# Performance work log

Hardware: AMD Instinct MI355X
Metric: run time of the kernel (lower is better)

Reference implementation:

```python
import jax, jax.numpy as jnp
import numpy as np

BN_EPS = 1e-5

def _segment_mean(vals, idx, num_segments):
    s = jax.ops.segment_sum(vals, idx, num_segments=num_segments)
    cnt = jax.ops.segment_sum(jnp.ones((vals.shape[0],), vals.dtype), idx, num_segments=num_segments)
    return s / jnp.maximum(cnt, 1.0)[:, None]


def setup_inputs() -> dict:
    N, E, L = 50000, 800000, 1600000
    ND, ED = 256, 128
    key = jax.random.key(0)
    ks = jax.random.split(key, 8)
    return {
        "x": jax.random.normal(ks[0], (N, ND), jnp.float32),
        "edge_attr": jax.random.normal(ks[1], (E, ED), jnp.float32),
        "W_proj": jax.random.normal(ks[2], (ED, ND), jnp.float32) / np.sqrt(ND),
        "W1": jax.random.normal(ks[3], (ED, ED), jnp.float32) / np.sqrt(ED),
        "b1": jnp.zeros((ED,), jnp.float32),
        "prelu_a": jnp.full((1,), 0.25, jnp.float32),
        "bn_gamma": jnp.ones((ED,), jnp.float32),
        "bn_beta": jnp.zeros((ED,), jnp.float32),
        "edge_index": jax.random.randint(ks[4], (2, E), 0, N, jnp.int32),
        "line_graph_edge_index": jax.random.randint(ks[5], (2, L), 0, E, jnp.int32),
    }


def reference(x, edge_attr, W_proj, W1, b1, prelu_a, bn_gamma, bn_beta, edge_index, line_graph_edge_index):
    N = x.shape[0]
    E = edge_attr.shape[0]
    src, dst = edge_index[0], edge_index[1]
    # project once then gather (same math as gathering then projecting)
    px = x @ W_proj.T  # [N, edge_dim]
    fused = edge_attr + (px[src] + px[dst]) * 0.5  # [E, edge_dim]
    # line-graph message passing: scatter-mean over destination edges
    line_src, line_dst = line_graph_edge_index[0], line_graph_edge_index[1]
    agg = _segment_mean(fused[line_src], line_dst, E)  # [E, edge_dim]
    # edge update: Linear -> PReLU -> BatchNorm1d (training-mode batch stats)
    h = agg @ W1.T + b1
    h = jnp.where(h >= 0, h, prelu_a * h)
    mean = jnp.mean(h, axis=0)
    var = jnp.mean(jnp.square(h - mean), axis=0)  # biased, as torch BN
    h = (h - mean) * jax.lax.rsqrt(var + BN_EPS) * bn_gamma + bn_beta
    fused = fused + h
    # aggregate edges back to nodes (scatter-mean over dst)
    node_updates = _segment_mean(fused, dst, N)  # [N, edge_dim]
    return node_updates
```

## Files before the change

kernel.cpp:

```cpp
#include <hip/hip_runtime.h>
#include <cstdint>

#define BN_EPS 1e-5f

typedef __attribute__((ext_vector_type(8))) short bf16x8;
typedef __attribute__((ext_vector_type(4))) float f32x4;

#define GLD16(dst, src)                                                        \
  __builtin_amdgcn_global_load_lds(                                            \
      (const __attribute__((address_space(1))) void*)(src),                    \
      (__attribute__((address_space(3))) void*)(dst), 16, 0, 0)

__device__ inline void split8(const float* f, bf16x8& hi, bf16x8& lo) {
#pragma unroll
  for (int j = 0; j < 8; ++j) {
    unsigned u = __float_as_uint(f[j]);
    hi[j] = (short)(u >> 16);
    float r = f[j] - __uint_as_float(u & 0xFFFF0000u);
    lo[j] = (short)(__float_as_uint(r) >> 16);
  }
}

template<int K, bool EPI>
__global__ __launch_bounds__(256) void gemm_kernel(
    const float* __restrict__ A,
    const float* __restrict__ W,
    const float* __restrict__ bias,
    const float* __restrict__ prelu_a,
    float* __restrict__ C,
    float* __restrict__ bnsum,
    float* __restrict__ bnsumsq,
    int M)
{
    constexpr int BM = 64, BN = 128, BK = 32;
    __shared__ float aT[BK][BM + 4];
    __shared__ float wT[BK][BN];

    const int tid = threadIdx.x;
    const int tx = tid & 31;
    const int ty = tid >> 5;
    const int row0 = blockIdx.x * BM;

    float acc[8][4];
#pragma unroll
    for (int r = 0; r < 8; ++r)
#pragma unroll
        for (int c = 0; c < 4; ++c) acc[r][c] = 0.f;

    for (int k0 = 0; k0 < K; k0 += BK) {
#pragma unroll
        for (int rep = 0; rep < 2; ++rep) {
            int r  = (tid >> 3) + rep * 32;
            int kq = tid & 7;
            int grow = row0 + r;
            float4 v = make_float4(0.f, 0.f, 0.f, 0.f);
            if (grow < M)
                v = *(const float4*)(A + (size_t)grow * K + k0 + 4 * kq);
            aT[4*kq+0][r] = v.x;
            aT[4*kq+1][r] = v.y;
            aT[4*kq+2][r] = v.z;
            aT[4*kq+3][r] = v.w;
        }
#pragma unroll
        for (int rep = 0; rep < 4; ++rep) {
            int j  = tid & 127;
            int kh = tid >> 7;
            int kk = kh * 16 + rep * 4;
            float4 v = *(const float4*)(W + (size_t)j * K + k0 + kk);
            wT[kk+0][j] = v.x;
            wT[kk+1][j] = v.y;
            wT[kk+2][j] = v.z;
            wT[kk+3][j] = v.w;
        }
        __syncthreads();
#pragma unroll
        for (int k = 0; k < BK; ++k) {
            float4 w4 = *(const float4*)&wT[k][4*tx];
            float4 a0 = *(const float4*)&aT[k][8*ty];
            float4 a1 = *(const float4*)&aT[k][8*ty+4];
            float av[8] = {a0.x,a0.y,a0.z,a0.w,a1.x,a1.y,a1.z,a1.w};
            float wv[4] = {w4.x,w4.y,w4.z,w4.w};
#pragma unroll
            for (int r = 0; r < 8; ++r)
#pragma unroll
                for (int c = 0; c < 4; ++c)
                    acc[r][c] = fmaf(av[r], wv[c], acc[r][c]);
        }
        __syncthreads();
    }

#pragma unroll
    for (int r = 0; r < 8; ++r) {
        int grow = row0 + 8*ty + r;
        if (grow < M) {
            float4 o = make_float4(acc[r][0], acc[r][1], acc[r][2], acc[r][3]);
            *(float4*)(C + (size_t)grow * BN + 4*tx) = o;
        }
    }
    (void)bias; (void)prelu_a; (void)bnsum; (void)bnsumsq;
}

__global__ __launch_bounds__(512, 1) void gemm_h_kernel(
    const float* __restrict__ A,
    const float* __restrict__ W,
    const float* __restrict__ bias,
    const float* __restrict__ prelu_a,
    float* __restrict__ C,
    float* __restrict__ bnsum, float* __restrict__ bnsumsq, int M)
{
    __shared__ float  Abuf[2][64 * 128];
    __shared__ bf16x8 Wh[32 * 64];
    __shared__ bf16x8 Wl[32 * 64];
    __shared__ float  red_s[128], red_q[128];

    const int tid = threadIdx.x;
    const int l   = tid & 63;
    const int w   = tid >> 6;
    const int rt  = w >> 1;
    const int ch  = w & 1;
    const int lr  = l & 15;
    const int ks  = l >> 4;

#pragma unroll
    for (int pp = 0; pp < 4; ++pp) {
        int p  = w * 4 + pp;
        int kc = p >> 3, n = p & 7;
        int col = n * 16 + lr;
        int k0  = kc * 32 + ks * 8;
        const float* wp = W + (size_t)col * 128 + k0;
        float f[8];
        *(float4*)&f[0] = *(const float4*)wp;
        *(float4*)&f[4] = *(const float4*)(wp + 4);
        bf16x8 hi, lo;
        split8(f, hi, lo);
        Wh[p * 64 + l] = hi;
        Wl[p * 64 + l] = lo;
    }

    const int T = (M + 63) / 64;
    const float pa = prelu_a[0];
    float b_c[4];
#pragma unroll
    for (int nn = 0; nn < 4; ++nn) b_c[nn] = bias[ch * 64 + nn * 16 + lr];

    float lsum[4] = {0.f,0.f,0.f,0.f}, lsq[4] = {0.f,0.f,0.f,0.f};

    const int t0 = blockIdx.x;
    const int G  = gridDim.x;

    auto stage = [&](int buf, int t) {
#pragma unroll
        for (int p = 0; p < 4; ++p) {
            int chunk = p * 512 + tid;
            int row   = chunk >> 5;
            long grow = (long)t * 64 + row;
            if (grow >= M) grow = M - 1;
            const char* src = (const char*)A + grow * 512 + (size_t)(chunk & 31) * 16;
            char* dst = (char*)&Abuf[buf][0] + (size_t)chunk * 16;
            GLD16(dst, src);
        }
    };

    if (t0 < T) stage(0, t0);
    __syncthreads();

    for (int i = 0, t = t0; t < T; ++i, t += G) {
        int cur = i & 1;
        int tn = t + G;
        if (tn < T) stage(cur ^ 1, tn);

        f32x4 acc[4];
#pragma unroll
        for (int nn = 0; nn < 4; ++nn) acc[nn] = (f32x4){0.f,0.f,0.f,0.f};

        const float* Ab = &Abuf[cur][0];
        const int r = rt * 16 + lr;
#pragma unroll
        for (int kc = 0; kc < 4; ++kc) {
            int seg = (kc * 4 + ks) ^ lr;
            const float* ap = Ab + r * 128 + seg * 8;
            float f[8];
            *(float4*)&f[0] = *(const float4*)ap;
            *(float4*)&f[4] = *(const float4*)(ap + 4);
            bf16x8 ah, al;
            split8(f, ah, al);
#pragma unroll
            for (int nn = 0; nn < 4; ++nn) {
                int p = kc * 8 + (ch * 4 + nn);
                bf16x8 bh = Wh[p * 64 + l];
                bf16x8 bl = Wl[p * 64 + l];
                acc[nn] = __builtin_amdgcn_mfma_f32_16x16x32_bf16(ah, bh, acc[nn], 0, 0, 0);
                acc[nn] = __builtin_amdgcn_mfma_f32_16x16x32_bf16(ah, bl, acc[nn], 0, 0, 0);
                acc[nn] = __builtin_amdgcn_mfma_f32_16x16x32_bf16(al, bh, acc[nn], 0, 0, 0);
            }
        }

#pragma unroll
        for (int nn = 0; nn < 4; ++nn) {
            int col = ch * 64 + nn * 16 + lr;
#pragma unroll
            for (int reg = 0; reg < 4; ++reg) {
                long grow = (long)t * 64 + rt * 16 + ks * 4 + reg;
                if (grow < M) {
                    float v = acc[nn][reg] + b_c[nn];
                    v = (v >= 0.f) ? v : pa * v;
                    C[grow * 128 + col] = v;
                    lsum[nn] += v;
                    lsq[nn]  += v * v;
                }
            }
        }
        __syncthreads();
    }

    if (tid < 128) { red_s[tid] = 0.f; red_q[tid] = 0.f; }
    __syncthreads();
#pragma unroll
    for (int nn = 0; nn < 4; ++nn) {
        int col = ch * 64 + nn * 16 + lr;
        atomicAdd(&red_s[col], lsum[nn]);
        atomicAdd(&red_q[col], lsq[nn]);
    }
    __syncthreads();
    if (tid < 128) {
        atomicAdd(&bnsum[tid],   red_s[tid]);
        atomicAdd(&bnsumsq[tid], red_q[tid]);
    }
}

__global__ __launch_bounds__(256) void fuse_kernel(
    const float* __restrict__ edge_attr, const float* __restrict__ px,
    const int* __restrict__ src, const int* __restrict__ dst,
    float* __restrict__ fused, int E)
{
    size_t i = (size_t)blockIdx.x * blockDim.x + threadIdx.x;
    size_t total = (size_t)E * 32;
    if (i >= total) return;
    int e = (int)(i >> 5);
    int q = (int)(i & 31);
    int s = src[e], d = dst[e];
    float4 ea = ((const float4*)edge_attr)[i];
    float4 ps = ((const float4*)px)[(size_t)s * 32 + q];
    float4 pd = ((const float4*)px)[(size_t)d * 32 + q];
    float4 o;
    o.x = ea.x + 0.5f * (ps.x + pd.x);
    o.y = ea.y + 0.5f * (ps.y + pd.y);
    o.z = ea.z + 0.5f * (ps.z + pd.z);
    o.w = ea.w + 0.5f * (ps.w + pd.w);
    ((float4*)fused)[i] = o;
}

__global__ __launch_bounds__(256) void hist_kernel(
    const int* __restrict__ idx, int* __restrict__ deg, int n)
{
    int i = blockIdx.x * 256 + threadIdx.x;
    if (i < n) atomicAdd(&deg[idx[i]], 1);
}

__global__ __launch_bounds__(256) void scan_local_kernel(
    const int* __restrict__ deg, int* __restrict__ excl,
    int* __restrict__ bsum, int n)
{
    __shared__ int ts[256];
    int t = threadIdx.x;
    int base = blockIdx.x * 2048 + t * 8;
    int v[8]; int s = 0;
#pragma unroll
    for (int j = 0; j < 8; ++j) { v[j] = (base + j < n) ? deg[base + j] : 0; s += v[j]; }
    ts[t] = s; __syncthreads();
    for (int off = 1; off < 256; off <<= 1) {
        int x = (t >= off) ? ts[t - off] : 0;
        __syncthreads();
        ts[t] += x;
        __syncthreads();
    }
    if (t == 255) bsum[blockIdx.x] = ts[255];
    int run = ts[t] - s;
#pragma unroll
    for (int j = 0; j < 8; ++j) {
        if (base + j < n) excl[base + j] = run;
        run += v[j];
    }
}

__global__ __launch_bounds__(256) void scan_blocks_kernel(int* __restrict__ bsum, int nb)
{
    __shared__ int ts[256];
    __shared__ int carry_s;
    int t = threadIdx.x;
    if (t == 0) carry_s = 0;
    __syncthreads();
    for (int c0 = 0; c0 < nb; c0 += 256) {
        int v = (c0 + t < nb) ? bsum[c0 + t] : 0;
        ts[t] = v; __syncthreads();
        for (int off = 1; off < 256; off <<= 1) {
            int x = (t >= off) ? ts[t - off] : 0;
            __syncthreads();
            ts[t] += x;
            __syncthreads();
        }
        int carry = carry_s;
        if (c0 + t < nb) bsum[c0 + t] = carry + ts[t] - v;
        int tot = ts[255];
        __syncthreads();
        if (t == 0) carry_s = carry + tot;
        __syncthreads();
    }
}

__global__ __launch_bounds__(256) void scan_add_kernel(
    int* __restrict__ rowptr, const int* __restrict__ bsum,
    int* __restrict__ cursor, int n, int total)
{
    int i = blockIdx.x * 256 + threadIdx.x;
    if (i == 0) rowptr[n] = total;
    if (i >= n) return;
    int v = rowptr[i] + bsum[i >> 11];
    rowptr[i] = v;
    cursor[i] = v;
}

__global__ __launch_bounds__(256) void fill_kernel(
    const int* __restrict__ dsti, const int* __restrict__ vals,
    int* __restrict__ cursor, int* __restrict__ adj, int n)
{
    int i = blockIdx.x * 256 + threadIdx.x;
    if (i >= n) return;
    int pos = atomicAdd(&cursor[dsti[i]], 1);
    adj[pos] = vals ? vals[i] : i;
}

__global__ __launch_bounds__(256) void gather_line_kernel(
    const float* __restrict__ fused, const int* __restrict__ rowptr,
    const int* __restrict__ adj, float* __restrict__ agg, int E)
{
    int w = (int)(((size_t)blockIdx.x * 256 + threadIdx.x) >> 6);
    int lane = threadIdx.x & 63;
    if (w >= E) return;
    int s0 = rowptr[w], s1 = rowptr[w + 1];
    int deg = s1 - s0;

    int myadj = (s0 + lane < s1) ? adj[s0 + lane] : 0;

    float2 acc = make_float2(0.f, 0.f);
    int cnt = min(deg, 64);
    for (int k = 0; k < cnt; k += 4) {
        int b  = cnt - k;
        int lastk = cnt - 1;
        int e0 = __shfl(myadj, k);
        int e1 = __shfl(myadj, min(k + 1, lastk));
        int e2 = __shfl(myadj, min(k + 2, lastk));
        int e3 = __shfl(myadj, min(k + 3, lastk));
        float2 v0 = ((const float2*)(fused + (size_t)e0 * 128))[lane];
        float2 v1 = ((const float2*)(fused + (size_t)e1 * 128))[lane];
        float2 v2 = ((const float2*)(fused + (size_t)e2 * 128))[lane];
        float2 v3 = ((const float2*)(fused + (size_t)e3 * 128))[lane];
        acc.x += v0.x; acc.y += v0.y;
        if (b > 1) { acc.x += v1.x; acc.y += v1.y; }
        if (b > 2) { acc.x += v2.x; acc.y += v2.y; }
        if (b > 3) { acc.x += v3.x; acc.y += v3.y; }
    }
    for (int j = s0 + 64; j < s1; ++j) {
        int e = adj[j];
        float2 v = ((const float2*)(fused + (size_t)e * 128))[lane];
        acc.x += v.x; acc.y += v.y;
    }

    float scl = 1.f / fmaxf((float)deg, 1.f);
    int seg = lane >> 2;
    int sw  = seg ^ (w & 15);
    *(float2*)((char*)agg + (size_t)w * 512 + ((size_t)sw << 5) + ((size_t)(lane & 3) << 3))
        = make_float2(acc.x * scl, acc.y * scl);
}

__global__ void bn_finalize_kernel(
    const float* __restrict__ bnsum, const float* __restrict__ bnsumsq,
    const float* __restrict__ gamma, const float* __restrict__ beta,
    float* __restrict__ cA, float* __restrict__ cB, float invE)
{
    int c = threadIdx.x;
    float mean = bnsum[c] * invE;
    float var  = bnsumsq[c] * invE - mean * mean;
    float istd = 1.f / sqrtf(var + BN_EPS);
    float a = istd * gamma[c];
    cA[c] = a;
    cB[c] = beta[c] - mean * a;
}

__global__ __launch_bounds__(256) void gather_node_kernel(
    const float* __restrict__ fused, const float* __restrict__ h,
    const int* __restrict__ rowptr, const int* __restrict__ adj,
    const float* __restrict__ cA, const float* __restrict__ cB,
    float* __restrict__ out, int N)
{
    int w = (int)(((size_t)blockIdx.x * 256 + threadIdx.x) >> 6);
    int lane = threadIdx.x & 63;
    if (w >= N) return;
    int s0 = rowptr[w], s1 = rowptr[w + 1];
    int deg = s1 - s0;
    float2 A = ((const float2*)cA)[lane];
    float2 B = ((const float2*)cB)[lane];

    float2 accf = make_float2(0.f, 0.f);
    float2 acch = make_float2(0.f, 0.f);

    for (int base = s0; base < s1; base += 64) {
        int chunk = min(s1 - base, 64);
        int myadj = (base + lane < s1) ? adj[base + lane] : 0;
        for (int k = 0; k < chunk; k += 4) {
            int b = chunk - k;
            int lastk = chunk - 1;
            int e0 = __shfl(myadj, k);
            int e1 = __shfl(myadj, min(k + 1, lastk));
            int e2 = __shfl(myadj, min(k + 2, lastk));
            int e3 = __shfl(myadj, min(k + 3, lastk));
            float2 f0 = ((const float2*)(fused + (size_t)e0 * 128))[lane];
            float2 h0 = ((const float2*)(h     + (size_t)e0 * 128))[lane];
            float2 f1 = ((const float2*)(fused + (size_t)e1 * 128))[lane];
            float2 h1 = ((const float2*)(h     + (size_t)e1 * 128))[lane];
            float2 f2 = ((const float2*)(fused + (size_t)e2 * 128))[lane];
            float2 h2 = ((const float2*)(h     + (size_t)e2 * 128))[lane];
            float2 f3 = ((const float2*)(fused + (size_t)e3 * 128))[lane];
            float2 h3 = ((const float2*)(h     + (size_t)e3 * 128))[lane];
            accf.x += f0.x; accf.y += f0.y; acch.x += h0.x; acch.y += h0.y;
            if (b > 1) { accf.x += f1.x; accf.y += f1.y; acch.x += h1.x; acch.y += h1.y; }
            if (b > 2) { accf.x += f2.x; accf.y += f2.y; acch.x += h2.x; acch.y += h2.y; }
            if (b > 3) { accf.x += f3.x; accf.y += f3.y; acch.x += h3.x; acch.y += h3.y; }
        }
    }

    float scl = 1.f / fmaxf((float)deg, 1.f);
    float2 o;
    o.x = (accf.x + fmaf(acch.x, A.x, (float)deg * B.x)) * scl;
    o.y = (accf.y + fmaf(acch.y, A.y, (float)deg * B.y)) * scl;
    ((float2*)(out + (size_t)w * 128))[lane] = o;
}

extern "C" void kernel_launch(void* const* d_in, const int* in_sizes, int n_in,
                              void* d_out, int out_size, void* d_ws, size_t ws_size,
                              hipStream_t stream) {
    const float* x     = (const float*)d_in[0];
    const float* ea    = (const float*)d_in[1];
    const float* Wp    = (const float*)d_in[2];
    const float* W1    = (const float*)d_in[3];
    const float* b1    = (const float*)d_in[4];
    const float* pa    = (const float*)d_in[5];
    const float* gamma = (const float*)d_in[6];
    const float* beta  = (const float*)d_in[7];
    const int*   ei    = (const int*)d_in[8];
    const int*   lg    = (const int*)d_in[9];

    const int ND = 256, ED = 128;
    const int N = in_sizes[0] / ND;
    const int E = in_sizes[1] / ED;
    const int L = in_sizes[9] / 2;
    const int* src  = ei;
    const int* dstI = ei + E;
    const int* ls   = lg;
    const int* ld   = lg + L;

    float* ws = (float*)d_ws;
    size_t off = 0;
    float* px    = ws + off; off += (size_t)N * ED;
    float* fused = ws + off; off += (size_t)E * ED;
    float* aggh  = ws + off; off += (size_t)E * ED;
    float* bnsum = ws + off; off += ED;
    float* bnsq  = ws + off; off += ED;
    float* cA    = ws + off; off += ED;
    float* cB    = ws + off; off += ED;

    int* iws = (int*)(ws + off);
    size_t ioff = 0;
    int* deg_l  = iws + ioff; ioff += E;
    int* rp_l   = iws + ioff; ioff += E + 1;
    int* adj_l  = iws + ioff; ioff += L;
    int* bs_l   = iws + ioff; ioff += 1024;
    int* deg_n  = iws + ioff; ioff += N;
    int* rp_n   = iws + ioff; ioff += N + 1;
    int* adj_n  = iws + ioff; ioff += E;
    int* bs_n   = iws + ioff; ioff += 1024;

    float* out = (float*)d_out;

    const int nb_l = (E + 2047) / 2048;
    const int nb_n = (N + 2047) / 2048;

    hipMemsetAsync(bnsum, 0, 2 * ED * sizeof(float), stream);
    hipMemsetAsync(deg_l, 0, (size_t)E * sizeof(int), stream);
    hipMemsetAsync(deg_n, 0, (size_t)N * sizeof(int), stream);

    gemm_kernel<256, false><<<(N + 63) / 64, 256, 0, stream>>>(
        x, Wp, nullptr, nullptr, px, nullptr, nullptr, N);

    {
        size_t tot = (size_t)E * 32;
        fuse_kernel<<<(int)((tot + 255) / 256), 256, 0, stream>>>(ea, px, src, dstI, fused, E);
    }

    hist_kernel<<<(L + 255) / 256, 256, 0, stream>>>(ld, deg_l, L);
    scan_local_kernel<<<nb_l, 256, 0, stream>>>(deg_l, rp_l, bs_l, E);
    scan_blocks_kernel<<<1, 256, 0, stream>>>(bs_l, nb_l);
    scan_add_kernel<<<(E + 255) / 256, 256, 0, stream>>>(rp_l, bs_l, deg_l, E, L);
    fill_kernel<<<(L + 255) / 256, 256, 0, stream>>>(ld, ls, deg_l, adj_l, L);

    hist_kernel<<<(E + 255) / 256, 256, 0, stream>>>(dstI, deg_n, E);
    scan_local_kernel<<<nb_n, 256, 0, stream>>>(deg_n, rp_n, bs_n, N);
    scan_blocks_kernel<<<1, 256, 0, stream>>>(bs_n, nb_n);
    scan_add_kernel<<<(N + 255) / 256, 256, 0, stream>>>(rp_n, bs_n, deg_n, N, E);
    fill_kernel<<<(E + 255) / 256, 256, 0, stream>>>(dstI, nullptr, deg_n, adj_n, E);

    gather_line_kernel<<<(E + 3) / 4, 256, 0, stream>>>(fused, rp_l, adj_l, aggh, E);

    gemm_h_kernel<<<256, 512, 0, stream>>>(aggh, W1, b1, pa, aggh, bnsum, bnsq, E);

    bn_finalize_kernel<<<1, 128, 0, stream>>>(bnsum, bnsq, gamma, beta, cA, cB, 1.f / (float)E);

    gather_node_kernel<<<(N + 3) / 4, 256, 0, stream>>>(fused, aggh, rp_n, adj_n, cA, cB, out, N);
}
```

Measured before the change: 1.711 ms.

## Fuse line-graph gather into the MFMA GEMM kernel via shared-memory staging

The separate gather_line kernel that wrote the mean-aggregated rows to global memory is removed. The persistent GEMM kernel now gathers each 64-row tile itself: every wave aggregates 8 destination edges, interleaving their neighbour loads, and writes the swizzled results into LDS, which the MFMA stage then consumes directly. This avoids writing and re-reading the E×128 agg buffer and saves a launch. In exchange, the gather runs on only 256 blocks of 512 threads with less latency hiding, the async double-buffered prefetch is gone, and waves idle on the highest-degree edge in each group of 8.

```diff
diff --git a/kernel.cpp b/kernel.cpp
--- a/kernel.cpp
+++ b/kernel.cpp
@@ -5,11 +5,6 @@
 
 typedef __attribute__((ext_vector_type(8))) short bf16x8;
 typedef __attribute__((ext_vector_type(4))) float f32x4;
-
-#define GLD16(dst, src)                                                        \
-  __builtin_amdgcn_global_load_lds(                                            \
-      (const __attribute__((address_space(1))) void*)(src),                    \
-      (__attribute__((address_space(3))) void*)(dst), 16, 0, 0)
 
 __device__ inline void split8(const float* f, bf16x8& hi, bf16x8& lo) {
 #pragma unroll
@@ -100,15 +95,17 @@
     (void)bias; (void)prelu_a; (void)bnsum; (void)bnsumsq;
 }
 
-__global__ __launch_bounds__(512, 1) void gemm_h_kernel(
-    const float* __restrict__ A,
+__global__ __launch_bounds__(512, 1) void gather_gemm_kernel(
+    const float* __restrict__ fused,
+    const int*   __restrict__ rowptr,
+    const int*   __restrict__ adj,
     const float* __restrict__ W,
     const float* __restrict__ bias,
     const float* __restrict__ prelu_a,
     float* __restrict__ C,
-    float* __restrict__ bnsum, float* __restrict__ bnsumsq, int M)
-{
-    __shared__ float  Abuf[2][64 * 128];
+    float* __restrict__ bnsum, float* __restrict__ bnsumsq, int E)
+{
+    __shared__ float  Abuf[64 * 128];
     __shared__ bf16x8 Wh[32 * 64];
     __shared__ bf16x8 Wl[32 * 64];
     __shared__ float  red_s[128], red_q[128];
@@ -137,7 +134,7 @@
         Wl[p * 64 + l] = lo;
     }
 
-    const int T = (M + 63) / 64;
+    const int T = (E + 63) / 64;
     const float pa = prelu_a[0];
     float b_c[4];
 #pragma unroll
@@ -145,40 +142,87 @@
 
     float lsum[4] = {0.f,0.f,0.f,0.f}, lsq[4] = {0.f,0.f,0.f,0.f};
 
-    const int t0 = blockIdx.x;
-    const int G  = gridDim.x;
-
-    auto stage = [&](int buf, int t) {
-#pragma unroll
-        for (int p = 0; p < 4; ++p) {
-            int chunk = p * 512 + tid;
-            int row   = chunk >> 5;
-            long grow = (long)t * 64 + row;
-            if (grow >= M) grow = M - 1;
-            const char* src = (const char*)A + grow * 512 + (size_t)(chunk & 31) * 16;
-            char* dst = (char*)&Abuf[buf][0] + (size_t)chunk * 16;
-            GLD16(dst, src);
-        }
-    };
-
-    if (t0 < T) stage(0, t0);
-    __syncthreads();
-
-    for (int i = 0, t = t0; t < T; ++i, t += G) {
-        int cur = i & 1;
-        int tn = t + G;
-        if (tn < T) stage(cur ^ 1, tn);
-
-        f32x4 acc[4];
-#pragma unroll
-        for (int nn = 0; nn < 4; ++nn) acc[nn] = (f32x4){0.f,0.f,0.f,0.f};
-
-        const float* Ab = &Abuf[cur][0];
+    for (int t = blockIdx.x; t < T; t += gridDim.x) {
+        const int ebase = t * 64 + w * 8;
+
+        int l9   = (l < 9) ? l : 8;
+        int ridx = ebase + l9;
+        if (ridx > E) ridx = E;
+        int rp   = rowptr[ridx];
+        int rp0  = __shfl(rp, 0);
+        int rp8  = __shfl(rp, 8);
+        int tot  = rp8 - rp0;
+
+        int dg[8], sx[8];
+        int maxdeg = 0;
+#pragma unroll
+        for (int i = 0; i < 8; ++i) {
+            int a = __shfl(rp, i);
+            int b = __shfl(rp, i + 1);
+            dg[i] = b - a;
+            sx[i] = a - rp0;
+            maxdeg = max(maxdeg, dg[i]);
+        }
+
+        int ac = (l < tot) ? adj[rp0 + l] : 0;
+
+        float2 acc[8];
+#pragma unroll
+        for (int i = 0; i < 8; ++i) acc[i] = make_float2(0.f, 0.f);
+
+        for (int s = 0; s < maxdeg; s += 2) {
+            float2 tA[8], tB[8];
+            const int haveB = (s + 1 < maxdeg);
+#pragma unroll
+            for (int i = 0; i < 8; ++i) {
+                int idx = sx[i] + s;
+                idx = min(idx, tot - 1);
+                int row = (idx < 64) ? __shfl(ac, idx) : adj[rp0 + idx];
+                tA[i] = ((const float2*)(fused + (size_t)row * 128))[l];
+            }
+            if (haveB) {
+#pragma unroll
+                for (int i = 0; i < 8; ++i) {
+                    int idx = sx[i] + s + 1;
+                    idx = min(idx, tot - 1);
+                    int row = (idx < 64) ? __shfl(ac, idx) : adj[rp0 + idx];
+                    tB[i] = ((const float2*)(fused + (size_t)row * 128))[l];
+                }
+            }
+#pragma unroll
+            for (int i = 0; i < 8; ++i) {
+                if (s < dg[i])     { acc[i].x += tA[i].x; acc[i].y += tA[i].y; }
+            }
+            if (haveB) {
+#pragma unroll
+                for (int i = 0; i < 8; ++i) {
+                    if (s + 1 < dg[i]) { acc[i].x += tB[i].x; acc[i].y += tB[i].y; }
+                }
+            }
+        }
+
+        __syncthreads();
+
+#pragma unroll
+        for (int i = 0; i < 8; ++i) {
+            int r = w * 8 + i;
+            float scl = 1.f / fmaxf((float)dg[i], 1.f);
+            int seg = l >> 2;
+            int sw  = seg ^ (r & 15);
+            *(float2*)((char*)Abuf + (size_t)r * 512 + (sw << 5) + ((l & 3) << 3))
+                = make_float2(acc[i].x * scl, acc[i].y * scl);
+        }
+        __syncthreads();
+
+        f32x4 macc[4];
+#pragma unroll
+        for (int nn = 0; nn < 4; ++nn) macc[nn] = (f32x4){0.f,0.f,0.f,0.f};
+
         const int r = rt * 16 + lr;
 #pragma unroll
         for (int kc = 0; kc < 4; ++kc) {
             int seg = (kc * 4 + ks) ^ lr;
-            const float* ap = Ab + r * 128 + seg * 8;
+            const float* ap = Abuf + r * 128 + seg * 8;
             float f[8];
             *(float4*)&f[0] = *(const float4*)ap;
             *(float4*)&f[4] = *(const float4*)(ap + 4);
@@ -189,9 +233,9 @@
                 int p = kc * 8 + (ch * 4 + nn);
                 bf16x8 bh = Wh[p * 64 + l];
                 bf16x8 bl = Wl[p * 64 + l];
-                acc[nn] = __builtin_amdgcn_mfma_f32_16x16x32_bf16(ah, bh, acc[nn], 0, 0, 0);
-                acc[nn] = __builtin_amdgcn_mfma_f32_16x16x32_bf16(ah, bl, acc[nn], 0, 0, 0);
-                acc[nn] = __builtin_amdgcn_mfma_f32_16x16x32_bf16(al, bh, acc[nn], 0, 0, 0);
+                macc[nn] = __builtin_amdgcn_mfma_f32_16x16x32_bf16(ah, bh, macc[nn], 0, 0, 0);
+                macc[nn] = __builtin_amdgcn_mfma_f32_16x16x32_bf16(ah, bl, macc[nn], 0, 0, 0);
+                macc[nn] = __builtin_amdgcn_mfma_f32_16x16x32_bf16(al, bh, macc[nn], 0, 0, 0);
             }
         }
 
@@ -201,8 +245,8 @@
 #pragma unroll
             for (int reg = 0; reg < 4; ++reg) {
                 long grow = (long)t * 64 + rt * 16 + ks * 4 + reg;
-                if (grow < M) {
-                    float v = acc[nn][reg] + b_c[nn];
+                if (grow < E) {
+                    float v = macc[nn][reg] + b_c[nn];
                     v = (v >= 0.f) ? v : pa * v;
                     C[grow * 128 + col] = v;
                     lsum[nn] += v;
@@ -210,7 +254,6 @@
                 }
             }
         }
-        __syncthreads();
     }
 
     if (tid < 128) { red_s[tid] = 0.f; red_q[tid] = 0.f; }
@@ -328,49 +371,6 @@
     if (i >= n) return;
     int pos = atomicAdd(&cursor[dsti[i]], 1);
     adj[pos] = vals ? vals[i] : i;
-}
-
-__global__ __launch_bounds__(256) void gather_line_kernel(
-    const float* __restrict__ fused, const int* __restrict__ rowptr,
-    const int* __restrict__ adj, float* __restrict__ agg, int E)
-{
-    int w = (int)(((size_t)blockIdx.x * 256 + threadIdx.x) >> 6);
-    int lane = threadIdx.x & 63;
-    if (w >= E) return;
-    int s0 = rowptr[w], s1 = rowptr[w + 1];
-    int deg = s1 - s0;
-
-    int myadj = (s0 + lane < s1) ? adj[s0 + lane] : 0;
-
-    float2 acc = make_float2(0.f, 0.f);
-    int cnt = min(deg, 64);
-    for (int k = 0; k < cnt; k += 4) {
-        int b  = cnt - k;
-        int lastk = cnt - 1;
-        int e0 = __shfl(myadj, k);
-        int e1 = __shfl(myadj, min(k + 1, lastk));
-        int e2 = __shfl(myadj, min(k + 2, lastk));
-        int e3 = __shfl(myadj, min(k + 3, lastk));
-        float2 v0 = ((const float2*)(fused + (size_t)e0 * 128))[lane];
-        float2 v1 = ((const float2*)(fused + (size_t)e1 * 128))[lane];
-        float2 v2 = ((const float2*)(fused + (size_t)e2 * 128))[lane];
-        float2 v3 = ((const float2*)(fused + (size_t)e3 * 128))[lane];
-        acc.x += v0.x; acc.y += v0.y;
-        if (b > 1) { acc.x += v1.x; acc.y += v1.y; }
-        if (b > 2) { acc.x += v2.x; acc.y += v2.y; }
-        if (b > 3) { acc.x += v3.x; acc.y += v3.y; }
-    }
-    for (int j = s0 + 64; j < s1; ++j) {
-        int e = adj[j];
-        float2 v = ((const float2*)(fused + (size_t)e * 128))[lane];
-        acc.x += v.x; acc.y += v.y;
-    }
-
-    float scl = 1.f / fmaxf((float)deg, 1.f);
-    int seg = lane >> 2;
-    int sw  = seg ^ (w & 15);
-    *(float2*)((char*)agg + (size_t)w * 512 + ((size_t)sw << 5) + ((size_t)(lane & 3) << 3))
-        = make_float2(acc.x * scl, acc.y * scl);
 }
 
 __global__ void bn_finalize_kernel(
@@ -509,9 +509,8 @@
     scan_add_kernel<<<(N + 255) / 256, 256, 0, stream>>>(rp_n, bs_n, deg_n, N, E);
     fill_kernel<<<(E + 255) / 256, 256, 0, stream>>>(dstI, nullptr, deg_n, adj_n, E);
 
-    gather_line_kernel<<<(E + 3) / 4, 256, 0, stream>>>(fused, rp_l, adj_l, aggh, E);
-
-    gemm_h_kernel<<<256, 512, 0, stream>>>(aggh, W1, b1, pa, aggh, bnsum, bnsq, E);
+    gather_gemm_kernel<<<256, 512, 0, stream>>>(
+        fused, rp_l, adj_l, W1, b1, pa, aggh, bnsum, bnsq, E);
 
     bn_finalize_kernel<<<1, 128, 0, stream>>>(bnsum, bnsq, gamma, beta, cA, cB, 1.f / (float)E);
 
```

Measured after the change: 2.114 ms. 1.24x slower.
